# Optimization experiments

Measured on AMD Instinct MI355X. Metric: run time of the kernel, lower is better.

## Reference

```python
import jax, jax.numpy as jnp
import numpy as np

B, S, D, H = 4, 2048, 512, 4


def setup_inputs() -> dict:
    key = jax.random.key(0)
    ks = jax.random.split(key, 12)
    sd = 1.0 / np.sqrt(D)
    def lin(k, i, o):
        return jax.random.uniform(k, (i, o), jnp.float32, -sd, sd)
    return {
        "fencs": jax.random.normal(ks[0], (B, S, D), jnp.float32),
        # per-head Q/K/V projections, stacked over H heads: [H, D, D] (+ bias [H, D])
        "Wq": jnp.stack([lin(jax.random.fold_in(ks[1], h), D, D) for h in range(H)]),
        "bq": jax.random.uniform(ks[2], (H, D), jnp.float32, -sd, sd),
        "Wk": jnp.stack([lin(jax.random.fold_in(ks[3], h), D, D) for h in range(H)]),
        "bk": jax.random.uniform(ks[4], (H, D), jnp.float32, -sd, sd),
        "Wv": jnp.stack([lin(jax.random.fold_in(ks[5], h), D, D) for h in range(H)]),
        "bv": jax.random.uniform(ks[6], (H, D), jnp.float32, -sd, sd),
        # FFN: dims -> 4*dims -> dims, residual
        "W1": lin(ks[7], D, 4 * D),
        "b1": jax.random.uniform(ks[8], (4 * D,), jnp.float32, -sd, sd),
        "W2": lin(ks[9], 4 * D, D),
        "b2": jax.random.uniform(ks[10], (D,), jnp.float32, -sd, sd),
    }


def reference(fencs, Wq, bq, Wk, bk, Wv, bv, W1, b1, W2, b2):
    d = fencs.shape[-1]
    scale = 1.0 / jnp.sqrt(jnp.asarray(d, fencs.dtype))
    # batched per-head projections: [B,H,S,D]
    q = jnp.einsum("bsd,hde->bhse", fencs, Wq) + bq[None, :, None, :]
    k = jnp.einsum("bsd,hde->bhse", fencs, Wk) + bk[None, :, None, :]
    v = jnp.einsum("bsd,hde->bhse", fencs, Wv) + bv[None, :, None, :]
    scores = jnp.einsum("bhse,bhte->bhst", q, k) * scale  # [B,H,S,S]
    probs = jax.nn.softmax(scores, axis=-1)
    ctx = jnp.einsum("bhst,bhte->bhse", probs, v)  # [B,H,S,D]
    att = jnp.mean(ctx, axis=1)  # sum over heads / nheads -> [B,S,D]
    # FFN with residual around the FFN (residual input is the attention output)
    hid = jax.nn.relu(att @ W1 + b1)
    return att + (hid @ W2 + b2)
```

## Files before the change

kernel.cpp:

```cpp
#include <hip/hip_runtime.h>
#include <hip/hip_bf16.h>

typedef __attribute__((ext_vector_type(8))) short bf16x8;
typedef __attribute__((ext_vector_type(4))) float f32x4;

constexpr int Bc = 4, Sc = 2048, Dc = 512, Hc = 4;
constexpr float SCALE = 0.044194173824159216f;

__device__ __forceinline__ unsigned short f2bf(float f) {
  union { float f; unsigned u; } v; v.f = f;
  unsigned r = v.u + 0x7fffu + ((v.u >> 16) & 1u);
  return (unsigned short)(r >> 16);
}

#define GLD16(GP, LP) __builtin_amdgcn_global_load_lds( \
    (const __attribute__((address_space(1))) unsigned int*)(GP), \
    (__attribute__((address_space(3))) unsigned int*)(LP), 16, 0, 0)

__global__ __launch_bounds__(256) void k_cvt(const float* __restrict__ x,
                                             unsigned short* __restrict__ y, int n4) {
  int i = blockIdx.x * 256 + threadIdx.x;
  if (i < n4) {
    float4 v = ((const float4*)x)[i];
    ushort4 o;
    o.x = f2bf(v.x); o.y = f2bf(v.y); o.z = f2bf(v.z); o.w = f2bf(v.w);
    ((ushort4*)y)[i] = o;
  }
}

__global__ __launch_bounds__(256) void k_zero(float* __restrict__ p, int n4) {
  int i = blockIdx.x * 256 + threadIdx.x;
  if (i < n4) ((float4*)p)[i] = float4{0.f, 0.f, 0.f, 0.f};
}

__global__ __launch_bounds__(256) void k_fin(const float* __restrict__ x,
                                             unsigned short* __restrict__ y, int n4) {
  int i = blockIdx.x * 256 + threadIdx.x;
  if (i < n4) {
    float4 v = ((const float4*)x)[i];
    ushort4 o;
    o.x = f2bf(v.x); o.y = f2bf(v.y); o.z = f2bf(v.z); o.w = f2bf(v.w);
    ((ushort4*)y)[i] = o;
  }
}

__global__ __launch_bounds__(256) void k_wt(const float* __restrict__ W,
                                            unsigned short* __restrict__ WT,
                                            int K_, int N_, float scale) {
  const int z = blockIdx.z;
  W  += (size_t)z * K_ * N_;
  WT += (size_t)z * K_ * N_;
  __shared__ float t[32][33];
  const int k0 = blockIdx.x * 32, n0 = blockIdx.y * 32;
  const int tx = threadIdx.x & 31, ty = threadIdx.x >> 5;
#pragma unroll
  for (int i = 0; i < 32; i += 8) t[ty + i][tx] = W[(size_t)(k0 + ty + i) * N_ + n0 + tx];
  __syncthreads();
#pragma unroll
  for (int i = 0; i < 32; i += 8)
    WT[(size_t)(n0 + ty + i) * K_ + k0 + tx] = f2bf(t[tx][ty + i] * scale);
}

enum { EPI_QKV = 0, EPI_EXP = 1, EPI_PV = 2, EPI_RELU = 3, EPI_OUT = 4 };

template <int EPI>
__global__ __launch_bounds__(256)
void k_gemm(const unsigned short* __restrict__ A, size_t sA,
            const unsigned short* __restrict__ BTg,
            const float* __restrict__ bias, const float* __restrict__ biasK,
            const float* __restrict__ biasV,
            void* __restrict__ outv, float* __restrict__ extra,
            int K, float bscale)
{
  const int tid = threadIdx.x;
  const int w = tid >> 6, l = tid & 63;
  const int l15 = l & 15, lg = l >> 4;
  const int mb = blockIdx.x * 128, nb = blockIdx.y * 128;
  const int z = blockIdx.z;
  int h, mat = 0;
  if constexpr (EPI == EPI_QKV) { mat = z >> 2; h = z & 3; }
  else h = z;
  const unsigned short* Ae = A + (size_t)h * sA;
  const unsigned short* Be;
  if constexpr (EPI == EPI_QKV)
    Be = BTg + (size_t)mat * 1048576 + (size_t)h * 262144;
  else
    Be = BTg + (size_t)h * (size_t)(gridDim.y * 128) * K;

  __shared__ __align__(16) unsigned short As0[128 * 64], As1[128 * 64];
  __shared__ __align__(16) unsigned short Bs0[128 * 64], Bs1[128 * 64];

  f32x4 acc[4][4] = {};
  const int wm = w >> 1, wn = w & 1;
  const int mw = wm * 64, nw = wn * 64;
  const int nkt = K >> 6;

  auto stage = [&](int kb, unsigned short* Ad, unsigned short* Bd) {
#pragma unroll
    for (int i = 0; i < 4; ++i) {
      const int chunk = (w * 4 + i) * 64 + l;
      const int row = chunk >> 3;
      const int sb = ((chunk & 7) * 16) ^ ((row & 7) << 4);
      GLD16(Ae + (size_t)(mb + row) * K + kb + (sb >> 1), (char*)Ad + (w * 4 + i) * 1024);
      GLD16(Be + (size_t)(nb + row) * K + kb + (sb >> 1), (char*)Bd + (w * 4 + i) * 1024);
    }
  };
  auto compute = [&](const unsigned short* Asb, const unsigned short* Bsb) {
#pragma unroll
    for (int ks = 0; ks < 2; ++ks) {
      bf16x8 af[4], bfr[4];
#pragma unroll
      for (int m = 0; m < 4; ++m) {
        const int row = mw + m * 16 + l15;
        const int off = (ks * 64 + lg * 16) ^ ((row & 7) << 4);
        af[m] = *(const bf16x8*)((const char*)Asb + row * 128 + off);
      }
#pragma unroll
      for (int n = 0; n < 4; ++n) {
        const int row = nw + n * 16 + l15;
        const int off = (ks * 64 + lg * 16) ^ ((row & 7) << 4);
        bfr[n] = *(const bf16x8*)((const char*)Bsb + row * 128 + off);
      }
#pragma unroll
      for (int m = 0; m < 4; ++m)
#pragma unroll
        for (int n = 0; n < 4; ++n)
          acc[m][n] = __builtin_amdgcn_mfma_f32_16x16x32_bf16(af[m], bfr[n], acc[m][n], 0, 0, 0);
    }
  };

  stage(0, As0, Bs0);
  __syncthreads();
  for (int kt = 0; kt < nkt; kt += 2) {
    if (kt + 1 < nkt) stage((kt + 1) << 6, As1, Bs1);
    compute(As0, Bs0);
    __syncthreads();
    if (kt + 2 < nkt) stage((kt + 2) << 6, As0, Bs0);
    compute(As1, Bs1);
    __syncthreads();
  }

  if constexpr (EPI == EPI_QKV) {
    const float* bs = (mat == 0) ? bias : (mat == 1) ? biasK : biasV;
    const float bm = (mat == 0) ? bscale : 1.0f;
    unsigned short* op = (unsigned short*)outv + (size_t)mat * 8388608;
#pragma unroll
    for (int m = 0; m < 4; ++m) {
#pragma unroll
      for (int n = 0; n < 4; ++n) {
        const int col = nb + nw + n * 16 + l15;
        const float bv = bs[h * Dc + col] * bm;
#pragma unroll
        for (int r = 0; r < 4; ++r) {
          const int row = mb + mw + m * 16 + lg * 4 + r;
          const float v = acc[m][n][r] + bv;
          const int bb = row >> 11, s = row & 2047;
          if (mat < 2)
            op[(((size_t)bb * Hc + h) * Sc + s) * Dc + col] = f2bf(v);
          else
            op[(((size_t)bb * Hc + h) * Dc + col) * Sc + s] = f2bf(v);
        }
      }
    }
  } else if constexpr (EPI == EPI_EXP) {
    unsigned short* P = (unsigned short*)outv;
#pragma unroll
    for (int m = 0; m < 4; ++m) {
#pragma unroll
      for (int r = 0; r < 4; ++r) {
        const int row = mb + mw + m * 16 + lg * 4 + r;
        float ps = 0.f;
#pragma unroll
        for (int n = 0; n < 4; ++n) {
          const int col = nb + nw + n * 16 + l15;
          const float p = __expf(acc[m][n][r]);
          ps += p;
          P[((size_t)h * Sc + row) * Sc + col] = f2bf(p);
        }
#pragma unroll
        for (int d = 1; d < 16; d <<= 1) ps += __shfl_xor(ps, d);
        if (l15 == 0) atomicAdd(&extra[h * Sc + row], ps);
      }
    }
  } else if constexpr (EPI == EPI_PV) {
    float* of = (float*)outv + (size_t)(h >> 2) * 1048576;
#pragma unroll
    for (int m = 0; m < 4; ++m) {
#pragma unroll
      for (int r = 0; r < 4; ++r) {
        const int row = mb + mw + m * 16 + lg * 4 + r;
        const float il = 0.25f / extra[h * Sc + row];
#pragma unroll
        for (int n = 0; n < 4; ++n) {
          const int col = nb + nw + n * 16 + l15;
          atomicAdd(&of[(size_t)row * Dc + col], acc[m][n][r] * il);
        }
      }
    }
  } else if constexpr (EPI == EPI_RELU) {
#pragma unroll
    for (int m = 0; m < 4; ++m) {
#pragma unroll
      for (int n = 0; n < 4; ++n) {
        const int col = nb + nw + n * 16 + l15;
        const float bv = bias[col];
#pragma unroll
        for (int r = 0; r < 4; ++r) {
          const int row = mb + mw + m * 16 + lg * 4 + r;
          ((unsigned short*)outv)[(size_t)row * 2048 + col] = f2bf(fmaxf(acc[m][n][r] + bv, 0.f));
        }
      }
    }
  } else {
    float* of = (float*)outv;
#pragma unroll
    for (int m = 0; m < 4; ++m) {
#pragma unroll
      for (int n = 0; n < 4; ++n) {
        const int col = nb + nw + n * 16 + l15;
        const float bv = bias[col];
#pragma unroll
        for (int r = 0; r < 4; ++r) {
          const int row = mb + mw + m * 16 + lg * 4 + r;
          of[(size_t)row * Dc + col] = acc[m][n][r] + bv + extra[(size_t)row * Dc + col];
        }
      }
    }
  }
}

extern "C" void kernel_launch(void* const* d_in, const int* in_sizes, int n_in,
                              void* d_out, int out_size, void* d_ws, size_t ws_size,
                              hipStream_t stream)
{
  const float* fencs = (const float*)d_in[0];
  const float* Wq  = (const float*)d_in[1];
  const float* bq  = (const float*)d_in[2];
  const float* Wk  = (const float*)d_in[3];
  const float* bk  = (const float*)d_in[4];
  const float* Wv  = (const float*)d_in[5];
  const float* bvv = (const float*)d_in[6];
  const float* W1  = (const float*)d_in[7];
  const float* b1  = (const float*)d_in[8];
  const float* W2  = (const float*)d_in[9];
  const float* b2  = (const float*)d_in[10];
  float* out = (float*)d_out;

  if (ws_size < 140574720u) return;
  unsigned short* Rw  = (unsigned short*)d_ws;
  unsigned short* WqT = Rw;
  unsigned short* WkT = Rw + (size_t)1048576;
  unsigned short* WvT = Rw + (size_t)2097152;
  unsigned short* Q2  = Rw + (size_t)3145728;
  unsigned short* K2  = Q2 + (size_t)8388608;
  unsigned short* VT2 = K2 + (size_t)8388608;
  unsigned short* P2  = VT2 + (size_t)8388608;
  float* attf = (float*)(P2 + (size_t)33554432);
  float* lbuf = attf + (size_t)4194304;
  unsigned short* Xp   = P2;
  unsigned short* attb = Q2;
  unsigned short* hid  = P2;
  unsigned short* W1T  = Rw;
  unsigned short* W2T  = Rw + (size_t)1048576;

  k_wt<<<dim3(16, 16, 4), 256, 0, stream>>>(Wq, WqT, 512, 512, SCALE);
  k_wt<<<dim3(16, 16, 4), 256, 0, stream>>>(Wk, WkT, 512, 512, 1.0f);
  k_wt<<<dim3(16, 16, 4), 256, 0, stream>>>(Wv, WvT, 512, 512, 1.0f);
  k_zero<<<4096, 256, 0, stream>>>(attf, 1048576);

  for (int p = 0; p < 2; ++p) {
    k_cvt<<<2048, 256, 0, stream>>>(fencs + (size_t)p * 2097152, Xp, 524288);
    k_gemm<EPI_QKV><<<dim3(32, 4, 12), 256, 0, stream>>>(
        Xp, 0, WqT, bq, bk, bvv, Q2, nullptr, 512, SCALE);
    k_zero<<<16, 256, 0, stream>>>(lbuf, 4096);
    k_gemm<EPI_EXP><<<dim3(16, 16, 8), 256, 0, stream>>>(
        Q2, 1048576, K2, nullptr, nullptr, nullptr, P2, lbuf, 512, 0.f);
    k_gemm<EPI_PV><<<dim3(16, 4, 8), 256, 0, stream>>>(
        P2, 4194304, VT2, nullptr, nullptr, nullptr,
        attf + (size_t)p * 2097152, lbuf, 2048, 0.f);
  }

  k_wt<<<dim3(16, 64, 1), 256, 0, stream>>>(W1, W1T, 512, 2048, 1.0f);
  k_wt<<<dim3(64, 16, 1), 256, 0, stream>>>(W2, W2T, 2048, 512, 1.0f);

  k_fin<<<4096, 256, 0, stream>>>(attf, attb, 1048576);

  k_gemm<EPI_RELU><<<dim3(64, 16, 1), 256, 0, stream>>>(
      attb, 0, W1T, b1, nullptr, nullptr, hid, nullptr, 512, 1.0f);
  k_gemm<EPI_OUT><<<dim3(64, 4, 1), 256, 0, stream>>>(
      hid, 0, W2T, b2, nullptr, nullptr, out, attf, 2048, 1.0f);
}
```

Baseline: 416.8 us.

## Fold Wq·Wkᵀ into one matrix and drop the K projection

Scores are rewritten as X·(Wq·Wkᵀ)·Xᵀ. A precomputed per-head 512x512 matrix M replaces separate Q and K projections. The query bias is folded into a bias vector (Wk·bq), and the key bias is dropped because it only adds a per-row constant that softmax cancels. K is no longer computed or stored: the score GEMM reads the bf16 input X directly as the B operand. This removes one third of the projection work and a K buffer write, at the cost of a small extra GEMM for M and some change in bf16 rounding behaviour.

```diff
diff --git a/kernel.cpp b/kernel.cpp
--- a/kernel.cpp
+++ b/kernel.cpp
@@ -18,12 +18,14 @@
     (__attribute__((address_space(3))) unsigned int*)(LP), 16, 0, 0)
 
 __global__ __launch_bounds__(256) void k_cvt(const float* __restrict__ x,
-                                             unsigned short* __restrict__ y, int n4) {
+                                             unsigned short* __restrict__ y, int n4,
+                                             float scale) {
   int i = blockIdx.x * 256 + threadIdx.x;
   if (i < n4) {
     float4 v = ((const float4*)x)[i];
     ushort4 o;
-    o.x = f2bf(v.x); o.y = f2bf(v.y); o.z = f2bf(v.z); o.w = f2bf(v.w);
+    o.x = f2bf(v.x * scale); o.y = f2bf(v.y * scale);
+    o.z = f2bf(v.z * scale); o.w = f2bf(v.w * scale);
     ((ushort4*)y)[i] = o;
   }
 }
@@ -61,31 +63,39 @@
     WT[(size_t)(n0 + ty + i) * K_ + k0 + tx] = f2bf(t[tx][ty + i] * scale);
 }
 
-enum { EPI_QKV = 0, EPI_EXP = 1, EPI_PV = 2, EPI_RELU = 3, EPI_OUT = 4 };
+__global__ __launch_bounds__(256) void k_vecmat(const float* __restrict__ bqv,
+                                                const float* __restrict__ Wk,
+                                                float* __restrict__ cvec) {
+  const int g = blockIdx.x * 256 + threadIdx.x;
+  const int h = g >> 9, d = g & 511;
+  const float* wr = Wk + ((size_t)h * 512 + d) * 512;
+  const float* bb = bqv + h * 512;
+  float s = 0.f;
+  for (int e = 0; e < 512; e += 4) {
+    const float4 w = *(const float4*)(wr + e);
+    const float4 q = *(const float4*)(bb + e);
+    s += w.x * q.x + w.y * q.y + w.z * q.z + w.w * q.w;
+  }
+  cvec[g] = s * SCALE;
+}
+
+enum { EPI_MT = 0, EPI_QK = 1, EPI_V = 2, EPI_EXP = 3, EPI_PV = 4, EPI_RELU = 5, EPI_OUT = 6 };
 
 template <int EPI>
 __global__ __launch_bounds__(256)
 void k_gemm(const unsigned short* __restrict__ A, size_t sA,
-            const unsigned short* __restrict__ BTg,
-            const float* __restrict__ bias, const float* __restrict__ biasK,
-            const float* __restrict__ biasV,
-            void* __restrict__ outv, float* __restrict__ extra,
-            int K, float bscale)
+            const unsigned short* __restrict__ BTg, size_t sB, int bzsh,
+            const float* __restrict__ bias,
+            void* __restrict__ outv, float* __restrict__ extra, int K)
 {
   const int tid = threadIdx.x;
   const int w = tid >> 6, l = tid & 63;
   const int l15 = l & 15, lg = l >> 4;
   const int mb = blockIdx.x * 128, nb = blockIdx.y * 128;
   const int z = blockIdx.z;
-  int h, mat = 0;
-  if constexpr (EPI == EPI_QKV) { mat = z >> 2; h = z & 3; }
-  else h = z;
-  const unsigned short* Ae = A + (size_t)h * sA;
-  const unsigned short* Be;
-  if constexpr (EPI == EPI_QKV)
-    Be = BTg + (size_t)mat * 1048576 + (size_t)h * 262144;
-  else
-    Be = BTg + (size_t)h * (size_t)(gridDim.y * 128) * K;
+  const int h = z;
+  const unsigned short* Ae = A + (size_t)z * sA;
+  const unsigned short* Be = BTg + (size_t)(z >> bzsh) * sB;
 
   __shared__ __align__(16) unsigned short As0[128 * 64], As1[128 * 64];
   __shared__ __align__(16) unsigned short Bs0[128 * 64], Bs1[128 * 64];
@@ -140,22 +150,33 @@
     __syncthreads();
   }
 
-  if constexpr (EPI == EPI_QKV) {
-    const float* bs = (mat == 0) ? bias : (mat == 1) ? biasK : biasV;
-    const float bm = (mat == 0) ? bscale : 1.0f;
-    unsigned short* op = (unsigned short*)outv + (size_t)mat * 8388608;
-#pragma unroll
-    for (int m = 0; m < 4; ++m) {
+  if constexpr (EPI == EPI_MT) {
+    unsigned short* op = (unsigned short*)outv;
+#pragma unroll
+    for (int m = 0; m < 4; ++m)
 #pragma unroll
       for (int n = 0; n < 4; ++n) {
         const int col = nb + nw + n * 16 + l15;
-        const float bv = bs[h * Dc + col] * bm;
+#pragma unroll
+        for (int r = 0; r < 4; ++r) {
+          const int row = mb + mw + m * 16 + lg * 4 + r;
+          op[((size_t)z * 512 + row) * 512 + col] = f2bf(acc[m][n][r]);
+        }
+      }
+  } else if constexpr (EPI == EPI_QK || EPI == EPI_V) {
+    unsigned short* op = (unsigned short*)outv;
+#pragma unroll
+    for (int m = 0; m < 4; ++m) {
+#pragma unroll
+      for (int n = 0; n < 4; ++n) {
+        const int col = nb + nw + n * 16 + l15;
+        const float bv = bias[h * Dc + col];
 #pragma unroll
         for (int r = 0; r < 4; ++r) {
           const int row = mb + mw + m * 16 + lg * 4 + r;
           const float v = acc[m][n][r] + bv;
           const int bb = row >> 11, s = row & 2047;
-          if (mat < 2)
+          if constexpr (EPI == EPI_QK)
             op[(((size_t)bb * Hc + h) * Sc + s) * Dc + col] = f2bf(v);
           else
             op[(((size_t)bb * Hc + h) * Dc + col) * Sc + s] = f2bf(v);
@@ -245,39 +266,46 @@
   const float* W2  = (const float*)d_in[9];
   const float* b2  = (const float*)d_in[10];
   float* out = (float*)d_out;
-
-  if (ws_size < 140574720u) return;
-  unsigned short* Rw  = (unsigned short*)d_ws;
-  unsigned short* WqT = Rw;
-  unsigned short* WkT = Rw + (size_t)1048576;
-  unsigned short* WvT = Rw + (size_t)2097152;
-  unsigned short* Q2  = Rw + (size_t)3145728;
-  unsigned short* K2  = Q2 + (size_t)8388608;
-  unsigned short* VT2 = K2 + (size_t)8388608;
-  unsigned short* P2  = VT2 + (size_t)8388608;
+  (void)bk;
+
+  if (ws_size < 134291456u) return;
+  unsigned short* MTb = (unsigned short*)d_ws;
+  unsigned short* WvT = MTb + (size_t)1048576;
+  unsigned short* W1T = WvT + (size_t)1048576;
+  unsigned short* W2T = W1T + (size_t)1048576;
+  unsigned short* Xbf = W2T + (size_t)1048576;
+  unsigned short* Qp  = Xbf + (size_t)4194304;
+  unsigned short* VTp = Qp  + (size_t)8388608;
+  unsigned short* P2  = VTp + (size_t)8388608;
   float* attf = (float*)(P2 + (size_t)33554432);
   float* lbuf = attf + (size_t)4194304;
-  unsigned short* Xp   = P2;
-  unsigned short* attb = Q2;
+  float* cvec = lbuf + (size_t)16384;
+  unsigned short* Wqs  = W1T;
+  unsigned short* Wkb  = W2T;
+  unsigned short* attb = Qp;
   unsigned short* hid  = P2;
-  unsigned short* W1T  = Rw;
-  unsigned short* W2T  = Rw + (size_t)1048576;
-
-  k_wt<<<dim3(16, 16, 4), 256, 0, stream>>>(Wq, WqT, 512, 512, SCALE);
-  k_wt<<<dim3(16, 16, 4), 256, 0, stream>>>(Wk, WkT, 512, 512, 1.0f);
+
+  k_cvt<<<4096, 256, 0, stream>>>(fencs, Xbf, 1048576, 1.0f);
+  k_cvt<<<1024, 256, 0, stream>>>(Wq, Wqs, 262144, SCALE);
+  k_cvt<<<1024, 256, 0, stream>>>(Wk, Wkb, 262144, 1.0f);
+  k_vecmat<<<8, 256, 0, stream>>>(bq, Wk, cvec);
+  k_gemm<EPI_MT><<<dim3(4, 4, 4), 256, 0, stream>>>(
+      Wkb, 262144, Wqs, 262144, 0, nullptr, MTb, nullptr, 512);
   k_wt<<<dim3(16, 16, 4), 256, 0, stream>>>(Wv, WvT, 512, 512, 1.0f);
   k_zero<<<4096, 256, 0, stream>>>(attf, 1048576);
 
   for (int p = 0; p < 2; ++p) {
-    k_cvt<<<2048, 256, 0, stream>>>(fencs + (size_t)p * 2097152, Xp, 524288);
-    k_gemm<EPI_QKV><<<dim3(32, 4, 12), 256, 0, stream>>>(
-        Xp, 0, WqT, bq, bk, bvv, Q2, nullptr, 512, SCALE);
+    const unsigned short* Xp = Xbf + (size_t)p * 2097152;
+    k_gemm<EPI_QK><<<dim3(32, 4, 4), 256, 0, stream>>>(
+        Xp, 0, MTb, 262144, 0, cvec, Qp, nullptr, 512);
+    k_gemm<EPI_V><<<dim3(32, 4, 4), 256, 0, stream>>>(
+        Xp, 0, WvT, 262144, 0, bvv, VTp, nullptr, 512);
     k_zero<<<16, 256, 0, stream>>>(lbuf, 4096);
     k_gemm<EPI_EXP><<<dim3(16, 16, 8), 256, 0, stream>>>(
-        Q2, 1048576, K2, nullptr, nullptr, nullptr, P2, lbuf, 512, 0.f);
+        Qp, 1048576, Xp, 1048576, 2, nullptr, P2, lbuf, 512);
     k_gemm<EPI_PV><<<dim3(16, 4, 8), 256, 0, stream>>>(
-        P2, 4194304, VT2, nullptr, nullptr, nullptr,
-        attf + (size_t)p * 2097152, lbuf, 2048, 0.f);
+        P2, 4194304, VTp, 1048576, 0, nullptr,
+        attf + (size_t)p * 2097152, lbuf, 2048);
   }
 
   k_wt<<<dim3(16, 64, 1), 256, 0, stream>>>(W1, W1T, 512, 2048, 1.0f);
@@ -286,7 +314,7 @@
   k_fin<<<4096, 256, 0, stream>>>(attf, attb, 1048576);
 
   k_gemm<EPI_RELU><<<dim3(64, 16, 1), 256, 0, stream>>>(
-      attb, 0, W1T, b1, nullptr, nullptr, hid, nullptr, 512, 1.0f);
+      attb, 0, W1T, 0, 0, b1, hid, nullptr, 512);
   k_gemm<EPI_OUT><<<dim3(64, 4, 1), 256, 0, stream>>>(
-      hid, 0, W2T, b2, nullptr, nullptr, out, attf, 2048, 1.0f);
-}
+      hid, 0, W2T, 0, 0, b2, out, attf, 2048);
+}
```

Measured after the change: 393.9 us, median of 2. -5.5%, faster.
